# Kernel optimization log

Hardware: AMD Instinct MI355X
Metric: run time of the kernel (lower is better)

The kernel has to match this reference:

```python
import jax, jax.numpy as jnp
import numpy as np
import math

NUM_HEADS = 8
DIM = 512

def setup_inputs() -> dict:
    key = jax.random.key(0)
    ks = jax.random.split(key, 10)
    t, b, a, f, d = 32, 64, 16, 128, DIM
    inp = {
        "q_embeds": jax.random.normal(ks[0], (t, b, a, d), dtype=jnp.float32),
        "context_embeds": jax.random.normal(ks[1], (t, f, b, d), dtype=jnp.float32),
        "attn_mask": jnp.ones((b, f), dtype=jnp.int32),
        "Wq": jax.random.normal(ks[2], (d, d), dtype=jnp.float32) / math.sqrt(d),
        "bq": jnp.zeros((d,), dtype=jnp.float32),
        "Wk": jax.random.normal(ks[3], (d, d), dtype=jnp.float32) / math.sqrt(d),
        "bk": jnp.zeros((d,), dtype=jnp.float32),
        "Wv": jax.random.normal(ks[4], (d, d), dtype=jnp.float32) / math.sqrt(d),
        "bv": jnp.zeros((d,), dtype=jnp.float32),
        "Wo": jax.random.normal(ks[5], (d, d), dtype=jnp.float32) / math.sqrt(d),
        "bo": jnp.zeros((d,), dtype=jnp.float32),
    }
    return inp

def reference(q_embeds, context_embeds, attn_mask, Wq, bq, Wk, bk, Wv, bv, Wo, bo):
    t, b, a, d = q_embeds.shape
    H = NUM_HEADS
    hd = d // H
    # q: (t,b,a,d) -> (t,b,H,hd,a)
    q = (q_embeds @ Wq.T + bq).reshape(t, b, a, H, hd).transpose(0, 1, 3, 4, 2)
    f = context_embeds.shape[1]
    # video_embeds: (t,f,b,d) -> (t,b,f,d)
    video_embeds = context_embeds.transpose(0, 2, 1, 3)
    # k_proj on (t,f,b,d) then raw reshape to (t,b,f,H,hd) -- faithful to torch .reshape
    k = (context_embeds @ Wk.T + bk).reshape(t, b, f, H, hd).transpose(0, 1, 3, 2, 4)  # (t,b,H,f,hd)
    v = (video_embeds @ Wv.T + bv).reshape(t, b, f, H, hd).transpose(0, 1, 3, 4, 2)   # (t,b,H,hd,f)
    logits = (k @ q) / math.sqrt(hd)  # (t,b,H,f,a)
    mask = attn_mask[None, :, None, :, None]  # (1,b,1,f,1)
    logits = jnp.where(mask == 0, jnp.float32(-1e9), logits)
    weights = jax.nn.softmax(logits, axis=-2)  # softmax over f
    attn = v @ weights  # (t,b,H,hd,a)
    attn = attn.transpose(0, 1, 4, 2, 3).reshape(t, b, a, d)
    o = attn @ Wo.T + bo  # (t,b,a,d)
    return (o.transpose(0, 2, 1, 3), weights)
```

## Files before the change

### kernel.cpp

```cpp
#include <hip/hip_runtime.h>
#include <hip/hip_bf16.h>

typedef __attribute__((ext_vector_type(8))) short short8;
typedef __attribute__((ext_vector_type(4))) float f32x4;

#define NT 32
#define NB 64
#define NA 16
#define NF 128
#define DT 512
#define NH 8
#define NHD 64

__device__ __forceinline__ unsigned short f2b(float f) {
  return __bfloat16_as_ushort(__float2bfloat16(f));
}
__device__ __forceinline__ float b2f(unsigned short u) {
  union { unsigned u; float f; } c; c.u = ((unsigned)u) << 16;
  return c.f;
}
__device__ __forceinline__ unsigned cvt2(float a, float b) {
  return (unsigned)f2b(a) | ((unsigned)f2b(b) << 16);
}

__device__ __forceinline__ void gload16(const void* g, void* l) {
  __builtin_amdgcn_global_load_lds(
      (const __attribute__((address_space(1))) void*)g,
      (__attribute__((address_space(3))) void*)l, 16, 0, 0);
}

#define BAR() asm volatile("s_barrier" ::: "memory")

__global__ __launch_bounds__(256) void cast4_kernel(const float* __restrict__ w0,
                                                    const float* __restrict__ w1,
                                                    const float* __restrict__ w2,
                                                    const float* __restrict__ w3,
                                                    unsigned short* __restrict__ dst) {
  const int mat = blockIdx.x >> 7;
  const float* src = (mat == 0) ? w0 : (mat == 1) ? w1 : (mat == 2) ? w2 : w3;
  long i = ((long)(blockIdx.x & 127) * 256 + threadIdx.x) * 8;
  float4 v0 = *(const float4*)(src + i);
  float4 v1 = *(const float4*)(src + i + 4);
  uint4 o;
  o.x = cvt2(v0.x, v0.y);
  o.y = cvt2(v0.z, v0.w);
  o.z = cvt2(v1.x, v1.y);
  o.w = cvt2(v1.z, v1.w);
  *(uint4*)(dst + (long)mat * 512 * 512 + i) = o;
}

template <int MODE, int NCB>
__global__ __launch_bounds__(256, 2) void gemm_f32a(const float* __restrict__ A,
                                                    const unsigned short* __restrict__ Bg,
                                                    const float* __restrict__ bias0,
                                                    const float* __restrict__ bias1,
                                                    unsigned short* __restrict__ C0,
                                                    unsigned short* __restrict__ C1) {
  __shared__ __align__(16) float Asf[2][128 * 32];
  __shared__ __align__(16) unsigned short Bsb[2][256 * 32];
  const int tid = threadIdx.x;
  const int lane = tid & 63;
  const int l4 = lane & 15, lg = lane >> 4;
  const int w = tid >> 6;
  const int wm = w >> 1, wn = w & 1;

  const int nwg = gridDim.x;
  const int bid = blockIdx.x;
  const int swz = (bid & 7) * (nwg >> 3) + (bid >> 3);
  const long rowTile = swz >> NCB;
  const int colTile = swz & ((1 << NCB) - 1);

  const int sA = (lane & 7) ^ ((lane >> 3) & 7);
  const float* AglB = A + (rowTile * 128 + w * 32 + (lane >> 3)) * 512L + sA * 4;
  const int sB = (lane & 3) ^ ((lane >> 3) & 3);
  const unsigned short* BglB = Bg + ((long)colTile * 256 + w * 64 + (lane >> 2)) * 512L + sB * 8;

  auto stage = [&](int s, int kc) {
#pragma unroll
    for (int j = 0; j < 4; j++)
      gload16(AglB + j * (8 * 512L) + kc, &Asf[s][w * 1024 + j * 256]);
#pragma unroll
    for (int j = 0; j < 4; j++)
      gload16(BglB + j * (16 * 512L) + kc, &Bsb[s][w * 2048 + j * 512]);
  };

  const f32x4 zero = {0.f, 0.f, 0.f, 0.f};
  f32x4 acc[4][8];
#pragma unroll
  for (int i = 0; i < 4; i++)
#pragma unroll
    for (int j = 0; j < 8; j++) acc[i][j] = zero;

  const int chA = (l4 & 7);
  const int chB = ((l4 >> 1) & 3);

  stage(0, 0);

#pragma unroll 1
  for (int T = 0; T < 16; T++) {
    const int s = T & 1;
    BAR();
    if (T < 15) {
      stage(s ^ 1, (T + 1) * 32);
      asm volatile("s_waitcnt vmcnt(8)" ::: "memory");
    } else {
      asm volatile("s_waitcnt vmcnt(0)" ::: "memory");
    }
    BAR();
    short8 bf[8];
#pragma unroll
    for (int n = 0; n < 8; n++) {
      int rb = wn * 128 + n * 16 + l4;
      bf[n] = *(const short8*)&Bsb[s][rb * 32 + (lg ^ chB) * 8];
    }
    short8 af[4];
#pragma unroll
    for (int m = 0; m < 4; m++) {
      int ra = wm * 64 + m * 16 + l4;
      int c0 = (lg * 2) ^ chA;
      f32x4 p0 = *(const f32x4*)&Asf[s][ra * 32 + c0 * 4];
      f32x4 p1 = *(const f32x4*)&Asf[s][ra * 32 + (c0 ^ 1) * 4];
      union { unsigned u[4]; short8 s8; } cv;
      cv.u[0] = cvt2(p0[0], p0[1]);
      cv.u[1] = cvt2(p0[2], p0[3]);
      cv.u[2] = cvt2(p1[0], p1[1]);
      cv.u[3] = cvt2(p1[2], p1[3]);
      af[m] = cv.s8;
    }
    __builtin_amdgcn_s_setprio(1);
#pragma unroll
    for (int m = 0; m < 4; m++)
#pragma unroll
      for (int n = 0; n < 8; n++)
        acc[m][n] = __builtin_amdgcn_mfma_f32_16x16x32_bf16(af[m], bf[n], acc[m][n], 0, 0, 0);
    __builtin_amdgcn_s_setprio(0);
  }

  const long rowBase = rowTile * 128 + wm * 64;

  if constexpr (MODE == 0) {
    if (colTile < 2) {
#pragma unroll
      for (int n = 0; n < 8; n++) {
        int gCol = colTile * 256 + wn * 128 + n * 16 + l4;
        float bs = bias0[gCol];
#pragma unroll
        for (int m = 0; m < 4; m++)
#pragma unroll
          for (int r = 0; r < 4; r++) {
            long gRow = rowBase + m * 16 + lg * 4 + r;
            C0[gRow * 512 + gCol] = f2b(acc[m][n][r] + bs);
          }
      }
    } else {
#pragma unroll
      for (int n = 0; n < 8; n++) {
        int gCol = (colTile - 2) * 256 + wn * 128 + n * 16 + l4;
        float bs = bias1[gCol];
#pragma unroll
        for (int m = 0; m < 4; m++)
#pragma unroll
          for (int r = 0; r < 4; r++) {
            long gRow = rowBase + m * 16 + lg * 4 + r;
            long rr = gRow & 8191;
            long vrow = (gRow - rr) + ((rr & 63) << 7) + (rr >> 6);
            C1[vrow * 512 + gCol] = f2b(acc[m][n][r] + bs);
          }
      }
    }
  } else {
#pragma unroll
    for (int n = 0; n < 8; n++) {
      int gCol = colTile * 256 + wn * 128 + n * 16 + l4;
      float bs = bias0[gCol];
#pragma unroll
      for (int m = 0; m < 4; m++)
#pragma unroll
        for (int r = 0; r < 4; r++) {
          long gRow = rowBase + m * 16 + lg * 4 + r;
          C0[gRow * 512 + gCol] = f2b(acc[m][n][r] + bs);
        }
    }
  }
}

__global__ __launch_bounds__(256) void gemm_o(const unsigned short* __restrict__ A,
                                              const unsigned short* __restrict__ Bg,
                                              const float* __restrict__ bias0,
                                              float* __restrict__ C) {
  __shared__ __align__(16) unsigned short As[128 * 32];
  __shared__ __align__(16) unsigned short Bs[128 * 32];
  const int tid = threadIdx.x;
  const int lane = tid & 63;
  const int l4 = lane & 15, lg = lane >> 4;
  const int w = tid >> 6;
  const int wm = w >> 1, wn = w & 1;

  const int nwg = gridDim.x;
  const int bid = blockIdx.x;
  const int swz = (bid & 7) * (nwg >> 3) + (bid >> 3);
  const long rowTile = swz >> 2;
  const int colTile = swz & 3;

  const int srow = lane >> 2;
  const int scol = (lane & 3) * 8;
  const unsigned short* Ab = A + (rowTile * 128 + w * 16 + srow) * 512L + scol;
  const unsigned short* Ab2 = Ab + 64 * 512L;
  const unsigned short* Bb = Bg + ((long)colTile * 128 + w * 16 + srow) * 512L + scol;
  const unsigned short* Bb2 = Bb + 64 * 512L;
  unsigned short* lA = As + w * 512;
  unsigned short* lA2 = As + (w + 4) * 512;
  unsigned short* lB = Bs + w * 512;
  unsigned short* lB2 = Bs + (w + 4) * 512;

  const f32x4 zero = {0.f, 0.f, 0.f, 0.f};
  f32x4 acc[4][4];
#pragma unroll
  for (int i = 0; i < 4; i++)
#pragma unroll
    for (int j = 0; j < 4; j++) acc[i][j] = zero;

  for (int k0 = 0; k0 < 512; k0 += 32) {
    gload16(Ab + k0, lA);
    gload16(Ab2 + k0, lA2);
    gload16(Bb + k0, lB);
    gload16(Bb2 + k0, lB2);
    __syncthreads();
    short8 af[4], bfr[4];
#pragma unroll
    for (int i = 0; i < 4; i++)
      af[i] = *(const short8*)(As + (wm * 64 + i * 16 + l4) * 32 + lg * 8);
#pragma unroll
    for (int j = 0; j < 4; j++)
      bfr[j] = *(const short8*)(Bs + (wn * 64 + j * 16 + l4) * 32 + lg * 8);
#pragma unroll
    for (int i = 0; i < 4; i++)
#pragma unroll
      for (int j = 0; j < 4; j++)
        acc[i][j] = __builtin_amdgcn_mfma_f32_16x16x32_bf16(af[i], bfr[j], acc[i][j], 0, 0, 0);
    __syncthreads();
  }

  const long rowBase = rowTile * 128 + wm * 64;
#pragma unroll
  for (int j = 0; j < 4; j++) {
    int gCol = colTile * 128 + wn * 64 + j * 16 + l4;
    float bs = bias0[gCol];
#pragma unroll
    for (int i = 0; i < 4; i++)
#pragma unroll
      for (int r = 0; r < 4; r++) {
        long gRow = rowBase + i * 16 + lg * 4 + r;
        long tt = gRow >> 10;
        long bi = (gRow >> 4) & 63;
        long ai = gRow & 15;
        long orow = ((tt * 16 + ai) << 6) + bi;
        C[orow * 512 + gCol] = acc[i][j][r] + bs;
      }
  }
}

__global__ __launch_bounds__(256) void attn_kernel(const unsigned short* __restrict__ Kst,
                                                   const unsigned short* __restrict__ Vst,
                                                   const unsigned short* __restrict__ Qst,
                                                   const int* __restrict__ mask,
                                                   float* __restrict__ wout,
                                                   unsigned short* __restrict__ attn_out) {
  __shared__ __align__(16) unsigned short wt[4][16][136];
  __shared__ __align__(16) unsigned short Vl[4][2][2048];
  __shared__ int msh[NF];
  const int tid = threadIdx.x;
  const int lane = tid & 63;
  const int l4 = lane & 15, lg = lane >> 4;
  const int w = tid >> 6;
  const int tb = blockIdx.x;
  const int b = tb & 63;
  if (tid < NF) msh[tid] = mask[b * NF + tid];
  __syncthreads();

  const unsigned short* Kbase = Kst + (long)tb * NF * DT;
  const unsigned short* Vbase = Vst + (long)tb * NF * DT;
  const unsigned short* Qbase = Qst + (long)tb * NA * DT;
  const f32x4 zero = {0.f, 0.f, 0.f, 0.f};

  const int vsr = lane >> 3;
  const int vsc = lane & 7;

  for (int hh = 0; hh < 2; hh++) {
    const int h = w * 2 + hh;
    const int co = h * 64;

    auto stageV = [&](int buf, int ks) {
#pragma unroll
      for (int i = 0; i < 4; i++) {
        const unsigned short* src =
            Vbase + (long)(ks * 32 + i * 8 + vsr) * DT + co + ((vsc ^ i) * 8);
        gload16(src, &Vl[w][buf][i * 512]);
      }
    };

    stageV(0, 0);

    f32x4 acc[8];
#pragma unroll
    for (int i = 0; i < 8; i++) acc[i] = zero;
#pragma unroll
    for (int ks = 0; ks < 2; ks++) {
      short8 qf = *(const short8*)(Qbase + (long)l4 * DT + co + ks * 32 + lg * 8);
#pragma unroll
      for (int m0 = 0; m0 < 8; m0++) {
        short8 kf = *(const short8*)(Kbase + (long)(m0 * 16 + l4) * DT + co + ks * 32 + lg * 8);
        acc[m0] = __builtin_amdgcn_mfma_f32_16x16x32_bf16(kf, qf, acc[m0], 0, 0, 0);
      }
    }
    float lv[8][4];
    float mx = -3.0e38f;
#pragma unroll
    for (int m0 = 0; m0 < 8; m0++)
#pragma unroll
      for (int r = 0; r < 4; r++) {
        int f = m0 * 16 + lg * 4 + r;
        float v = acc[m0][r] * 0.125f;
        if (msh[f] == 0) v = -1.0e9f;
        lv[m0][r] = v;
        mx = fmaxf(mx, v);
      }
    mx = fmaxf(mx, __shfl_xor(mx, 16, 64));
    mx = fmaxf(mx, __shfl_xor(mx, 32, 64));
    float s = 0.f;
#pragma unroll
    for (int m0 = 0; m0 < 8; m0++)
#pragma unroll
      for (int r = 0; r < 4; r++) {
        float p = __expf(lv[m0][r] - mx);
        lv[m0][r] = p;
        s += p;
      }
    s += __shfl_xor(s, 16, 64);
    s += __shfl_xor(s, 32, 64);
    float inv = 1.0f / s;
    float* wrow = wout + ((long)tb * NH + h) * (NF * NA);
#pragma unroll
    for (int m0 = 0; m0 < 8; m0++)
#pragma unroll
      for (int r = 0; r < 4; r++) {
        int f = m0 * 16 + lg * 4 + r;
        float wv = lv[m0][r] * inv;
        wrow[f * 16 + l4] = wv;
        wt[w][l4][f] = f2b(wv);
      }
    asm volatile("s_waitcnt lgkmcnt(0)" ::: "memory");
    __builtin_amdgcn_sched_barrier(0);

    f32x4 pacc[4];
#pragma unroll
    for (int m0 = 0; m0 < 4; m0++) pacc[m0] = zero;
    int vb = 0;
#pragma unroll 1
    for (int ks = 0; ks < 4; ks++) {
      if (ks < 3) {
        stageV(vb ^ 1, ks + 1);
        asm volatile("s_waitcnt vmcnt(4)" ::: "memory");
      } else {
        asm volatile("s_waitcnt vmcnt(0)" ::: "memory");
      }
      short8 wf = *(const short8*)&wt[w][l4][ks * 32 + lg * 8];
#pragma unroll
      for (int m0 = 0; m0 < 4; m0++) {
        const int hdl = m0 * 16 + l4;
        const int ch = ((hdl >> 3) ^ lg) & 7;
        const int cb = ch * 8 + (hdl & 7);
        short8 vf;
#pragma unroll
        for (int j = 0; j < 8; j++)
          vf[j] = (short)Vl[w][vb][(lg * 8 + j) * 64 + cb];
        pacc[m0] = __builtin_amdgcn_mfma_f32_16x16x32_bf16(vf, wf, pacc[m0], 0, 0, 0);
      }
      vb ^= 1;
    }
#pragma unroll
    for (int m0 = 0; m0 < 4; m0++)
#pragma unroll
      for (int r = 0; r < 4; r++)
        attn_out[((long)tb * NA + l4) * DT + co + m0 * 16 + lg * 4 + r] = f2b(pacc[m0][r]);
  }
}

extern "C" void kernel_launch(void* const* d_in, const int* in_sizes, int n_in,
                              void* d_out, int out_size, void* d_ws, size_t ws_size,
                              hipStream_t stream) {
  const float* q_embeds = (const float*)d_in[0];
  const float* ctx = (const float*)d_in[1];
  const int* mask = (const int*)d_in[2];
  const float* Wq = (const float*)d_in[3];
  const float* bq = (const float*)d_in[4];
  const float* Wk = (const float*)d_in[5];
  const float* bk = (const float*)d_in[6];
  const float* Wv = (const float*)d_in[7];
  const float* bv = (const float*)d_in[8];
  const float* Wo = (const float*)d_in[9];
  const float* bo = (const float*)d_in[10];

  float* out0 = (float*)d_out;
  float* wout = out0 + (long)NT * NA * NB * DT;

  const long W_ELEMS = 4L * 512 * 512;
  const long MQ = (long)NT * NB * NA;
  const long MKV = (long)NT * NF * NB;
  unsigned short* Wb = (unsigned short*)d_ws;
  unsigned short* Qst = Wb + W_ELEMS;
  unsigned short* Kst = Qst + MQ * DT;
  unsigned short* Vst = Kst + MKV * DT;
  unsigned short* attnst = Vst + MKV * DT;
  size_t needed = (size_t)(W_ELEMS + 2 * MQ * DT + 2 * MKV * DT) * 2;
  if (ws_size < needed) return;

  cast4_kernel<<<512, 256, 0, stream>>>(Wq, Wk, Wv, Wo, Wb);

  gemm_f32a<1, 1><<<(unsigned)(MQ / 128 * 2), 256, 0, stream>>>(
      q_embeds, Wb, bq, nullptr, Qst, nullptr);

  gemm_f32a<0, 2><<<(unsigned)(MKV / 128 * 4), 256, 0, stream>>>(
      ctx, Wb + 512 * 512, bk, bv, Kst, Vst);

  attn_kernel<<<NT * NB, 256, 0, stream>>>(Kst, Vst, Qst, mask, wout, attnst);

  gemm_o<<<(unsigned)(MQ / 128 * 4), 256, 0, stream>>>(attnst, Wb + 3 * 512 * 512, bo, out0);
}
```

Before: 750.8 us.

## Stage K tiles through LDS with a double-buffered async pipeline shared with V

The QK^T phase now loads K from global memory asynchronously into the per-wave LDS double buffer in 32-row slices, instead of reading K fragments straight from global memory. The K and V staging form one continuous prefetch pipeline: the last K slices overlap with prefetching the first V slices, and V prefetch runs two slices ahead. This is meant to hide global-load latency behind the score MFMAs and to get coalesced swizzled loads. The cost is more LDS traffic and waitcnt synchronisation that depends on the exact count of outstanding vmcnt operations.

```diff
diff --git a/kernel.cpp b/kernel.cpp
--- a/kernel.cpp
+++ b/kernel.cpp
@@ -290,29 +290,42 @@
     const int h = w * 2 + hh;
     const int co = h * 64;
 
-    auto stageV = [&](int buf, int ks) {
+    auto stageS = [&](const unsigned short* base, int buf, int sl) {
 #pragma unroll
       for (int i = 0; i < 4; i++) {
         const unsigned short* src =
-            Vbase + (long)(ks * 32 + i * 8 + vsr) * DT + co + ((vsc ^ i) * 8);
+            base + (long)(sl * 32 + i * 8 + vsr) * DT + co + ((vsc ^ i) * 8);
         gload16(src, &Vl[w][buf][i * 512]);
       }
     };
 
-    stageV(0, 0);
+    short8 qf0 = *(const short8*)(Qbase + (long)l4 * DT + co + lg * 8);
+    short8 qf1 = *(const short8*)(Qbase + (long)l4 * DT + co + 32 + lg * 8);
+    stageS(Kbase, 0, 0);
+    stageS(Kbase, 1, 1);
 
     f32x4 acc[8];
 #pragma unroll
     for (int i = 0; i < 8; i++) acc[i] = zero;
 #pragma unroll
-    for (int ks = 0; ks < 2; ks++) {
-      short8 qf = *(const short8*)(Qbase + (long)l4 * DT + co + ks * 32 + lg * 8);
-#pragma unroll
-      for (int m0 = 0; m0 < 8; m0++) {
-        short8 kf = *(const short8*)(Kbase + (long)(m0 * 16 + l4) * DT + co + ks * 32 + lg * 8);
-        acc[m0] = __builtin_amdgcn_mfma_f32_16x16x32_bf16(kf, qf, acc[m0], 0, 0, 0);
-      }
-    }
+    for (int mh = 0; mh < 4; mh++) {
+      const int buf = mh & 1;
+      asm volatile("s_waitcnt vmcnt(4)" ::: "memory");
+#pragma unroll
+      for (int mm = 0; mm < 2; mm++) {
+        const int m0 = mh * 2 + mm;
+        const int r = mm * 16 + l4;
+        short8 kf0 = *(const short8*)&Vl[w][buf][r * 64 + ((lg ^ (r >> 3)) * 8)];
+        short8 kf1 = *(const short8*)&Vl[w][buf][r * 64 + (((4 + lg) ^ (r >> 3)) * 8)];
+        acc[m0] = __builtin_amdgcn_mfma_f32_16x16x32_bf16(kf0, qf0, acc[m0], 0, 0, 0);
+        acc[m0] = __builtin_amdgcn_mfma_f32_16x16x32_bf16(kf1, qf1, acc[m0], 0, 0, 0);
+      }
+      asm volatile("s_waitcnt lgkmcnt(0)" ::: "memory");
+      __builtin_amdgcn_sched_barrier(0);
+      if (mh < 2) stageS(Kbase, buf, mh + 2);
+      else stageS(Vbase, buf, mh - 2);
+    }
+
     float lv[8][4];
     float mx = -3.0e38f;
 #pragma unroll
@@ -355,15 +368,13 @@
     f32x4 pacc[4];
 #pragma unroll
     for (int m0 = 0; m0 < 4; m0++) pacc[m0] = zero;
-    int vb = 0;
 #pragma unroll 1
     for (int ks = 0; ks < 4; ks++) {
-      if (ks < 3) {
-        stageV(vb ^ 1, ks + 1);
+      const int buf = ks & 1;
+      if (ks < 3)
         asm volatile("s_waitcnt vmcnt(4)" ::: "memory");
-      } else {
+      else
         asm volatile("s_waitcnt vmcnt(0)" ::: "memory");
-      }
       short8 wf = *(const short8*)&wt[w][l4][ks * 32 + lg * 8];
 #pragma unroll
       for (int m0 = 0; m0 < 4; m0++) {
@@ -373,10 +384,14 @@
         short8 vf;
 #pragma unroll
         for (int j = 0; j < 8; j++)
-          vf[j] = (short)Vl[w][vb][(lg * 8 + j) * 64 + cb];
+          vf[j] = (short)Vl[w][buf][(lg * 8 + j) * 64 + cb];
         pacc[m0] = __builtin_amdgcn_mfma_f32_16x16x32_bf16(vf, wf, pacc[m0], 0, 0, 0);
       }
-      vb ^= 1;
+      if (ks < 2) {
+        asm volatile("s_waitcnt lgkmcnt(0)" ::: "memory");
+        __builtin_amdgcn_sched_barrier(0);
+        stageS(Vbase, buf, ks + 2);
+      }
     }
 #pragma unroll
     for (int m0 = 0; m0 < 4; m0++)
```

Measured after the change: 735.8 us, median of 2. 1.02x faster.
